# Kernel optimization log

Hardware: AMD Instinct MI355X
Metric: run time of the kernel (lower is better)

The kernel has to match this reference:

```python
import jax, jax.numpy as jnp
import numpy as np

B, S, DIM = 2, 2048, 2048
H, KVH, HD = 16, 8, 128
NREP = H // KVH


def _make_freqs(seqlen, head_dim):
    # Rotation-matrix form of RoPE: freqs[s,0,p] = [[cos,-sin],[sin,cos]]
    pos = jnp.arange(seqlen, dtype=jnp.float32)
    inv = 1.0 / (10000.0 ** (jnp.arange(0, head_dim, 2, dtype=jnp.float32) / head_dim))
    ang = pos[:, None] * inv[None, :]                      # (S, HD/2)
    cos, sin = jnp.cos(ang), jnp.sin(ang)
    f = jnp.stack([jnp.stack([cos, -sin], -1),
                   jnp.stack([sin, cos], -1)], -2)          # (S, HD/2, 2, 2)
    return f[:, None]                                       # (S, 1, HD/2, 2, 2)


def setup_inputs() -> dict:
    key = jax.random.key(0)
    k0, k1, k2, k3, k4 = jax.random.split(key, 5)
    x = jax.random.normal(k0, (B, S, DIM), jnp.float32)
    x_mask = jnp.ones((B, S), jnp.bool_)                    # unused by forward
    freqs_cis = _make_freqs(S, HD)
    w_qkv = jax.random.normal(k1, ((H + 2 * KVH) * HD, DIM), jnp.float32) * (DIM ** -0.5)
    w_out = jax.random.normal(k2, (DIM, H * HD), jnp.float32) * ((H * HD) ** -0.5)
    q_norm_w = 1.0 + 0.02 * jax.random.normal(k3, (HD,), jnp.float32)
    k_norm_w = 1.0 + 0.02 * jax.random.normal(k4, (HD,), jnp.float32)
    return {"x": x, "x_mask": x_mask, "freqs_cis": freqs_cis,
            "w_qkv": w_qkv, "w_out": w_out,
            "q_norm_w": q_norm_w, "k_norm_w": k_norm_w}


def _rmsnorm(x, w):
    eps = jnp.asarray(jnp.finfo(x.dtype).eps, x.dtype)
    return x * jax.lax.rsqrt(jnp.mean(x * x, -1, keepdims=True) + eps) * w


def _rope(x, freqs):
    # x: (B,S,h,HD), freqs: (S,1,HD/2,2,2)
    t = x.reshape(*x.shape[:-1], HD // 2, 1, 2)
    out = freqs[..., 0] * t[..., 0] + freqs[..., 1] * t[..., 1]
    return out.reshape(x.shape)


def reference(x, x_mask, freqs_cis, w_qkv, w_out, q_norm_w, k_norm_w):
    b, s, _ = x.shape
    qkv = jnp.einsum('bsd,od->bso', x, w_qkv)
    xq, xk, xv = jnp.split(qkv, [H * HD, (H + KVH) * HD], axis=-1)
    xq = _rope(_rmsnorm(xq.reshape(b, s, H, HD), q_norm_w), freqs_cis)
    xk = _rope(_rmsnorm(xk.reshape(b, s, KVH, HD), k_norm_w), freqs_cis)
    xv = xv.reshape(b, s, KVH, HD)
    # GQA: repeat kv heads (consecutive copies, matching unsqueeze+repeat+flatten)
    xk = jnp.repeat(xk, NREP, axis=2)
    xv = jnp.repeat(xv, NREP, axis=2)
    scale = HD ** -0.5
    scores = jnp.einsum('bqhd,bkhd->bhqk', xq, xk) * scale
    attn = jax.nn.softmax(scores, axis=-1)
    out = jnp.einsum('bhqk,bkhd->bqhd', attn, xv).reshape(b, s, H * HD)
    return jnp.einsum('bso,do->bsd', out, w_out)
```

## Files before the change

kernel.cpp:

```cpp
#include <hip/hip_runtime.h>
#include <hip/hip_bf16.h>
#include <cstdint>

typedef __bf16 bf16_t;
typedef __attribute__((ext_vector_type(8)))  __bf16 bf16x8;
typedef __attribute__((ext_vector_type(4)))  float  f32x4;
typedef __attribute__((ext_vector_type(16))) float  f32x16;

#define AS1 __attribute__((address_space(1)))
#define AS3 __attribute__((address_space(3)))
#define DEV __device__ __forceinline__

#define S_BARRIER() asm volatile("s_barrier" ::: "memory")
#define VMCNT0()    asm volatile("s_waitcnt vmcnt(0)" ::: "memory")
#define VMCNT8()    asm volatile("s_waitcnt vmcnt(8)" ::: "memory")
#define SCHED0()    __builtin_amdgcn_sched_barrier(0)

#if __has_builtin(__builtin_amdgcn_exp2f)
#define EXP2(x) __builtin_amdgcn_exp2f(x)
#else
#define EXP2(x) exp2f(x)
#endif

DEV uint32_t pk2bf(float lo, float hi) {
  union { __bf16 h[2]; uint32_t u; } x;
  x.h[0] = (__bf16)lo; x.h[1] = (__bf16)hi; return x.u;
}

__global__ __launch_bounds__(256) void k_cvt3(const float* __restrict__ s0,
                                              const float* __restrict__ s1,
                                              const float* __restrict__ s2,
                                              bf16_t* __restrict__ dst) {
  long i = (long)(blockIdx.x * 256 + threadIdx.x) * 4;
  const float* src;
  long off;
  if (i < 8388608)        { src = s0; off = i; }
  else if (i < 16777216)  { src = s1; off = i - 8388608; }
  else                    { src = s2; off = i - 16777216; }
  const float4 v = *reinterpret_cast<const float4*>(src + off);
  union { bf16_t h[4]; uint2 u; } o;
  o.h[0] = (bf16_t)v.x; o.h[1] = (bf16_t)v.y;
  o.h[2] = (bf16_t)v.z; o.h[3] = (bf16_t)v.w;
  *reinterpret_cast<uint2*>(dst + i) = o.u;
}

#define RD_A_PAIR(dst, base, MF)                                          \
  _Pragma("unroll") for (int j_ = 0; j_ < 2; ++j_)                        \
  _Pragma("unroll") for (int kk_ = 0; kk_ < 2; ++kk_) {                   \
    int p_ = (wm*128 + ((MF)+j_)*16 + c16)*128 + kk_*64 + g*16;           \
    p_ ^= ((p_>>9)&1)<<5;                                                 \
    dst[j_][kk_] = *reinterpret_cast<const bf16x8*>((const char*)(base) + p_); }

#define RD_B_ALL(dst, base)                                               \
  _Pragma("unroll") for (int i_ = 0; i_ < 4; ++i_)                        \
  _Pragma("unroll") for (int kk_ = 0; kk_ < 2; ++kk_) {                   \
    int p_ = (wn*64 + i_*16 + c16)*128 + kk_*64 + g*16;                   \
    p_ ^= ((p_>>9)&1)<<5;                                                 \
    dst[i_][kk_] = *reinterpret_cast<const bf16x8*>((const char*)(base) + p_); }

#define RD_B2(dst, base)                                                  \
  _Pragma("unroll") for (int i_ = 0; i_ < 2; ++i_)                        \
  _Pragma("unroll") for (int kk_ = 0; kk_ < 2; ++kk_) {                   \
    int p_ = (wn*32 + i_*16 + c16)*128 + kk_*64 + g*16;                   \
    p_ ^= ((p_>>9)&1)<<5;                                                 \
    dst[i_][kk_] = *reinterpret_cast<const bf16x8*>((const char*)(base) + p_); }

#define MM_PAIR(aa, MF)                                                   \
  _Pragma("unroll") for (int j_ = 0; j_ < 2; ++j_)                        \
  _Pragma("unroll") for (int i_ = 0; i_ < 4; ++i_)                        \
  _Pragma("unroll") for (int kk_ = 0; kk_ < 2; ++kk_)                     \
    acc[(MF)+j_][i_] = __builtin_amdgcn_mfma_f32_16x16x32_bf16(           \
        aa[j_][kk_], bF[i_][kk_], acc[(MF)+j_][i_], 0, 0, 0);

#define MM_PAIR2(aa, MF)                                                  \
  _Pragma("unroll") for (int j_ = 0; j_ < 2; ++j_)                        \
  _Pragma("unroll") for (int i_ = 0; i_ < 2; ++i_)                        \
  _Pragma("unroll") for (int kk_ = 0; kk_ < 2; ++kk_)                     \
    acc[(MF)+j_][i_] = __builtin_amdgcn_mfma_f32_16x16x32_bf16(           \
        aa[j_][kk_], bG[i_][kk_], acc[(MF)+j_][i_], 0, 0, 0);

#define STAGE_A(dstbase, half, tt)                                        \
  _Pragma("unroll") for (int j_ = 0; j_ < 2; ++j_)                        \
    __builtin_amdgcn_global_load_lds(                                     \
        (const AS1 void*)(Ag + srcA[half][j_] + (tt)*64),                 \
        (AS3 void*)((char*)(dstbase) + ((half)*1024 + 512*j_ + wuni)*16), \
        16, 0, 0);

#define STAGE_B(dstbase, half, tt)                                        \
  _Pragma("unroll") for (int j_ = 0; j_ < 2; ++j_)                        \
    __builtin_amdgcn_global_load_lds(                                     \
        (const AS1 void*)(Bg + srcB[half][j_] + (tt)*64),                 \
        (AS3 void*)((char*)(dstbase) + ((half)*1024 + 512*j_ + wuni)*16), \
        16, 0, 0);

#define STAGE_B2(dstbase, tt)                                             \
  _Pragma("unroll") for (int j_ = 0; j_ < 2; ++j_)                        \
    __builtin_amdgcn_global_load_lds(                                     \
        (const AS1 void*)(Bg + srcB2[j_] + (tt)*64),                      \
        (AS3 void*)((char*)(dstbase) + (512*j_ + wuni)*16), 16, 0, 0);

__global__ __launch_bounds__(512, 2) void k_gemm256(
    const bf16_t* __restrict__ Ag, const bf16_t* __restrict__ Bg,
    void* __restrict__ Cv, int M, int N, int K, int out_bf16)
{
  extern __shared__ char smemraw[];
  const int tid = threadIdx.x;
  const int w = tid >> 6, l = tid & 63;
  const int wm = w >> 2, wn = w & 3;
  const int c16 = l & 15, g = l >> 4;
  const int wuni = tid & 0x1C0;

  const int nwg = gridDim.x, cpx = nwg >> 3;
  const int bid = blockIdx.x;
  const int L = (bid & 7) * cpx + (bid >> 3);
  const int nbx = N >> 8;
  const int m0 = (L / nbx) * 256, n0 = (L % nbx) * 256;

  int srcA[2][2], srcB[2][2];
#pragma unroll
  for (int half = 0; half < 2; ++half)
#pragma unroll
    for (int j = 0; j < 2; ++j) {
      int ch = half * 1024 + 512 * j + tid;
      int cc = ch ^ (((ch >> 5) & 1) << 1);
      int row = cc >> 3, c8 = (cc & 7) * 8;
      srcA[half][j] = (m0 + row) * K + c8;
      srcB[half][j] = (n0 + row) * K + c8;
    }

  f32x4 acc[8][4] = {};
  bf16x8 aA[2][2], aB[2][2], bF[4][2];

  char* const Ab0 = smemraw;
  char* const Ab1 = smemraw + 32768;
  char* const Bb0 = smemraw + 65536;
  char* const Bb1 = smemraw + 98304;

  const int NT = K >> 6;

  STAGE_A(Ab0, 0, 0); STAGE_A(Ab0, 1, 0);
  STAGE_B(Bb0, 0, 0); STAGE_B(Bb0, 1, 0);
  VMCNT0();
  S_BARRIER();
  RD_A_PAIR(aA, Ab0, 0);
  RD_B_ALL(bF, Bb0);

#pragma unroll 1
  for (int t = 0; t < NT; ++t) {
    char* const Asp = (t & 1) ? Ab1 : Ab0;
    char* const Asn = (t & 1) ? Ab0 : Ab1;
    char* const Bsn = (t & 1) ? Bb0 : Bb1;
    const bool more = (t + 1 < NT);

    RD_A_PAIR(aB, Asp, 2);
    if (more) { STAGE_A(Asn, 0, t + 1); STAGE_A(Asn, 1, t + 1); }
    S_BARRIER();
    __builtin_amdgcn_s_setprio(1);
    MM_PAIR(aA, 0);
    __builtin_amdgcn_s_setprio(0); SCHED0();
    S_BARRIER();

    RD_A_PAIR(aA, Asp, 4);
    if (more) { STAGE_B(Bsn, 0, t + 1); STAGE_B(Bsn, 1, t + 1); }
    S_BARRIER();
    __builtin_amdgcn_s_setprio(1);
    MM_PAIR(aB, 2);
    __builtin_amdgcn_s_setprio(0); SCHED0();
    S_BARRIER();

    RD_A_PAIR(aB, Asp, 6);
    S_BARRIER();
    __builtin_amdgcn_s_setprio(1);
    MM_PAIR(aA, 4);
    __builtin_amdgcn_s_setprio(0); SCHED0();
    S_BARRIER();

    if (more) { VMCNT0(); }
    S_BARRIER();
    __builtin_amdgcn_s_setprio(1);
    MM_PAIR(aB, 6);
    __builtin_amdgcn_s_setprio(0); SCHED0();
    if (more) { RD_A_PAIR(aA, Asn, 0); RD_B_ALL(bF, Bsn); }
    S_BARRIER();
  }

#pragma unroll
  for (int mf = 0; mf < 8; ++mf)
#pragma unroll
    for (int nf = 0; nf < 4; ++nf) {
      const int cc = n0 + wn * 64 + nf * 16 + c16;
#pragma unroll
      for (int r = 0; r < 4; ++r) {
        const int rr = m0 + wm * 128 + mf * 16 + g * 4 + r;
        if (out_bf16)
          ((bf16_t*)Cv)[(size_t)rr * N + cc] = (bf16_t)acc[mf][nf][r];
        else
          ((float*)Cv)[(size_t)rr * N + cc] = acc[mf][nf][r];
      }
    }
}

__global__ __launch_bounds__(512, 2) void k_og(
    const bf16_t* __restrict__ Ag, const bf16_t* __restrict__ Bg,
    float* __restrict__ Cv, int M, int N, int K)
{
  extern __shared__ char smemraw[];
  const int tid = threadIdx.x;
  const int w = tid >> 6, l = tid & 63;
  const int wm = w >> 2, wn = w & 3;
  const int c16 = l & 15, g = l >> 4;
  const int wuni = tid & 0x1C0;

  const int nwg = gridDim.x, cpx = nwg >> 3;
  const int bid = blockIdx.x;
  const int L = (bid & 7) * cpx + (bid >> 3);
  const int nbx = N >> 7;
  const int m0 = (L / nbx) * 256, n0 = (L % nbx) * 128;

  int srcA[2][2], srcB2[2];
#pragma unroll
  for (int half = 0; half < 2; ++half)
#pragma unroll
    for (int j = 0; j < 2; ++j) {
      int ch = half * 1024 + 512 * j + tid;
      int cc = ch ^ (((ch >> 5) & 1) << 1);
      int row = cc >> 3, c8 = (cc & 7) * 8;
      srcA[half][j] = (m0 + row) * K + c8;
    }
#pragma unroll
  for (int j = 0; j < 2; ++j) {
    int ch = 512 * j + tid;
    int cc = ch ^ (((ch >> 5) & 1) << 1);
    int row = cc >> 3, c8 = (cc & 7) * 8;
    srcB2[j] = (n0 + row) * K + c8;
  }

  f32x4 acc[8][2] = {};
  bf16x8 aA[2][2], aB[2][2], bG[2][2];

  char* const Ab0 = smemraw;
  char* const Ab1 = smemraw + 32768;
  char* const Bb0 = smemraw + 65536;
  char* const Bb1 = smemraw + 81920;

  const int NT = K >> 6;

  STAGE_A(Ab0, 0, 0); STAGE_A(Ab0, 1, 0);
  STAGE_B2(Bb0, 0);
  VMCNT0();
  S_BARRIER();
  RD_A_PAIR(aA, Ab0, 0);
  RD_B2(bG, Bb0);

#pragma unroll 1
  for (int t = 0; t < NT; ++t) {
    char* const Asp = (t & 1) ? Ab1 : Ab0;
    char* const Asn = (t & 1) ? Ab0 : Ab1;
    char* const Bsn = (t & 1) ? Bb0 : Bb1;
    const bool more = (t + 1 < NT);

    RD_A_PAIR(aB, Asp, 2);
    if (more) { STAGE_A(Asn, 0, t + 1); STAGE_A(Asn, 1, t + 1); }
    S_BARRIER();
    __builtin_amdgcn_s_setprio(1);
    MM_PAIR2(aA, 0);
    __builtin_amdgcn_s_setprio(0); SCHED0();
    S_BARRIER();

    RD_A_PAIR(aA, Asp, 4);
    if (more) { STAGE_B2(Bsn, t + 1); }
    S_BARRIER();
    __builtin_amdgcn_s_setprio(1);
    MM_PAIR2(aB, 2);
    __builtin_amdgcn_s_setprio(0); SCHED0();
    S_BARRIER();

    RD_A_PAIR(aB, Asp, 6);
    S_BARRIER();
    __builtin_amdgcn_s_setprio(1);
    MM_PAIR2(aA, 4);
    __builtin_amdgcn_s_setprio(0); SCHED0();
    S_BARRIER();

    if (more) { VMCNT0(); }
    S_BARRIER();
    __builtin_amdgcn_s_setprio(1);
    MM_PAIR2(aB, 6);
    __builtin_amdgcn_s_setprio(0); SCHED0();
    if (more) { RD_A_PAIR(aA, Asn, 0); RD_B2(bG, Bsn); }
    S_BARRIER();
  }

#pragma unroll
  for (int mf = 0; mf < 8; ++mf)
#pragma unroll
    for (int nf = 0; nf < 2; ++nf) {
      const int cc = n0 + wn * 32 + nf * 16 + c16;
#pragma unroll
      for (int r = 0; r < 4; ++r) {
        const int rr = m0 + wm * 128 + mf * 16 + g * 4 + r;
        Cv[(size_t)rr * N + cc] = acc[mf][nf][r];
      }
    }
}

__global__ __launch_bounds__(256) void k_prep(
    const bf16_t* __restrict__ qkv, const float* __restrict__ freqs,
    const float* __restrict__ qw, const float* __restrict__ kw,
    bf16_t* __restrict__ Qd, bf16_t* __restrict__ Kd,
    bf16_t* __restrict__ Vt)
{
  __shared__ bf16_t vt[64][136];
  const int bid = blockIdx.x;
  if (bid < 24576) {
    const int w = threadIdx.x >> 6, l = threadIdx.x & 63;
    const int R = bid * 4 + w;
    const int j = R >> 12;
    const int token = R & 4095;
    const int s = token & 2047, b = token >> 11;
    const bool isq = (j < 16);
    const int col0 = isq ? (j << 7) : (2048 + ((j - 16) << 7));

    union { uint32_t u; __bf16 h[2]; } xin;
    xin.u = *reinterpret_cast<const uint32_t*>(qkv + (size_t)token * 4096 + col0 + 2 * l);
    float x0 = (float)xin.h[0], x1 = (float)xin.h[1];
    float ss = x0 * x0 + x1 * x1;
#pragma unroll
    for (int d = 1; d < 64; d <<= 1) ss += __shfl_xor(ss, d, 64);
    const float rn = rsqrtf(ss * (1.0f / 128.0f) + 1.1920929e-7f);
    const float2 wv = *reinterpret_cast<const float2*>((isq ? qw : kw) + 2 * l);
    const float y0 = x0 * rn * wv.x, y1 = x1 * rn * wv.y;
    const float4 f = *reinterpret_cast<const float4*>(freqs + (size_t)s * 256 + l * 4);
    float o0 = f.x * y0 + f.y * y1;
    float o1 = f.z * y0 + f.w * y1;
    if (isq) { o0 *= 0.1275187989014331f; o1 *= 0.1275187989014331f; }
    const uint32_t pk = pk2bf(o0, o1);
    if (isq)
      *reinterpret_cast<uint32_t*>(Qd + ((size_t)(b * 16 + j) * 2048 + s) * 128 + 2 * l) = pk;
    else
      *reinterpret_cast<uint32_t*>(Kd + ((size_t)(b * 8 + (j - 16)) * 2048 + s) * 128 + 2 * l) = pk;
  } else {
    const int vb = bid - 24576;
    const int tid = threadIdx.x;
    const int st = vb & 31, kh = (vb >> 5) & 7, b = vb >> 8;
    const int s0 = st * 64;
#pragma unroll
    for (int i = 0; i < 4; ++i) {
      int ch = tid + 256 * i;
      int srow = ch >> 4, d8 = ch & 15;
      bf16x8 v = *reinterpret_cast<const bf16x8*>(
          qkv + (size_t)(b * 2048 + s0 + srow) * 4096 + 3072 + kh * 128 + d8 * 8);
      *reinterpret_cast<bf16x8*>(&vt[srow][d8 * 8]) = v;
    }
    __syncthreads();
    const int d = tid >> 1, sc = tid & 1;
    bf16_t* dst = Vt + ((size_t)(b * 8 + kh) * 128 + d) * 2048 + s0 + 32 * sc;
#pragma unroll
    for (int grp = 0; grp < 4; ++grp) {
      uint32_t pk[4];
#pragma unroll
      for (int q = 0; q < 4; ++q) {
        int jj = 32 * sc + grp * 8 + q * 2;
        union { __bf16 h[2]; uint32_t u; } e;
        e.h[0] = vt[jj][d]; e.h[1] = vt[jj + 1][d];
        pk[q] = e.u;
      }
      uint4 o; o.x = pk[0]; o.y = pk[1]; o.z = pk[2]; o.w = pk[3];
      *reinterpret_cast<uint4*>(dst + grp * 8) = o;
    }
  }
}

__global__ __launch_bounds__(256, 2) void k_attn(
    const bf16_t* __restrict__ Qd, const bf16_t* __restrict__ Kd,
    const bf16_t* __restrict__ Vt, bf16_t* __restrict__ O)
{
  __shared__ bf16_t kbuf[2][64 * 128];
  __shared__ bf16_t vbuf[2][128 * 64];
  const int tid = threadIdx.x;
  const int w = tid >> 6, l = tid & 63;
  const int c = l & 31, h2 = l >> 5;
  const int bid = blockIdx.x;
  const int qt = bid & 15, h = (bid >> 4) & 15, b = bid >> 8;
  const int kvh = h >> 1;
  const bf16_t* Qg = Qd + ((size_t)(b * 16 + h) * 2048 + qt * 128 + w * 32) * 128;
  const bf16_t* Kg = Kd + ((size_t)(b * 8 + kvh) * 2048) * 128;
  const bf16_t* Vg = Vt + ((size_t)(b * 8 + kvh) * 128) * 2048;

  bf16x8 qf[8];
#pragma unroll
  for (int s = 0; s < 8; ++s)
    qf[s] = *reinterpret_cast<const bf16x8*>(Qg + (size_t)c * 128 + s * 16 + h2 * 8);

  f32x16 oacc[4] = {};
  float l0 = 0.f, l1 = 0.f, l2 = 0.f, l3 = 0.f;

  auto stage = [&](int buf, int kt) {
#pragma unroll
    for (int i = 0; i < 4; ++i) {
      int ch = tid + 256 * i;
      {
        int key = ch >> 4, d16 = ch & 15;
        int soff = key * 256 + ((d16 * 16) ^ ((key & 7) << 4));
        __builtin_amdgcn_global_load_lds(
            (const AS1 void*)((const char*)Kg + (size_t)kt * 64 * 256 + soff),
            (AS3 void*)((char*)&kbuf[buf][0] + (w * 64 + 256 * i) * 16), 16, 0, 0);
      }
      {
        int d = ch >> 3, k8 = (ch & 7) ^ (d & 7);
        __builtin_amdgcn_global_load_lds(
            (const AS1 void*)(Vg + (size_t)d * 2048 + kt * 64 + k8 * 8),
            (AS3 void*)((char*)&vbuf[buf][0] + (w * 64 + 256 * i) * 16), 16, 0, 0);
      }
    }
  };

  auto compute = [&](int buf) {
    f32x16 sacc[2] = {};
    const char* kb = (const char*)&kbuf[buf][0];
    __builtin_amdgcn_s_setprio(1);
#pragma unroll
    for (int m = 0; m < 2; ++m)
#pragma unroll
      for (int s = 0; s < 8; ++s) {
        int byte = (m * 32 + c) * 256 + ((s * 32 + h2 * 16) ^ ((c & 7) << 4));
        bf16x8 kf = *reinterpret_cast<const bf16x8*>(kb + byte);
        sacc[m] = __builtin_amdgcn_mfma_f32_32x32x16_bf16(kf, qf[s], sacc[m], 0, 0, 0);
      }
    __builtin_amdgcn_s_setprio(0);

#pragma unroll
    for (int m = 0; m < 2; ++m)
#pragma unroll
      for (int r = 0; r < 16; r += 4) {
        float p0 = EXP2(sacc[m][r + 0]);
        float p1 = EXP2(sacc[m][r + 1]);
        float p2 = EXP2(sacc[m][r + 2]);
        float p3 = EXP2(sacc[m][r + 3]);
        sacc[m][r + 0] = p0; sacc[m][r + 1] = p1;
        sacc[m][r + 2] = p2; sacc[m][r + 3] = p3;
        l0 += p0; l1 += p1; l2 += p2; l3 += p3;
      }

    const char* vb = (const char*)&vbuf[buf][0];
#pragma unroll
    for (int t = 0; t < 4; ++t) {
      const int m = t >> 1, q2i = t & 1;
      uint32_t u0 = pk2bf(sacc[m][8 * q2i + 0], sacc[m][8 * q2i + 1]);
      uint32_t u1 = pk2bf(sacc[m][8 * q2i + 2], sacc[m][8 * q2i + 3]);
      uint32_t u2 = pk2bf(sacc[m][8 * q2i + 4], sacc[m][8 * q2i + 5]);
      uint32_t u3 = pk2bf(sacc[m][8 * q2i + 6], sacc[m][8 * q2i + 7]);
      auto r02 = __builtin_amdgcn_permlane32_swap((int)u0, (int)u2, false, false);
      auto r13 = __builtin_amdgcn_permlane32_swap((int)u1, (int)u3, false, false);
      union { uint32_t u[4]; bf16x8 v; } pb;
      pb.u[0] = (uint32_t)r02[0]; pb.u[1] = (uint32_t)r13[0];
      pb.u[2] = (uint32_t)r02[1]; pb.u[3] = (uint32_t)r13[1];
      __builtin_amdgcn_s_setprio(1);
#pragma unroll
      for (int df = 0; df < 4; ++df) {
        int byte = (df * 32 + c) * 128 + ((t * 32 + h2 * 16) ^ ((c & 7) << 4));
        bf16x8 vf = *reinterpret_cast<const bf16x8*>(vb + byte);
        oacc[df] = __builtin_amdgcn_mfma_f32_32x32x16_bf16(vf, pb.v, oacc[df], 0, 0, 0);
      }
      __builtin_amdgcn_s_setprio(0);
    }
  };

  stage(0, 0);
#pragma unroll 1
  for (int kt = 0; kt < 31; ++kt) {
    stage((kt + 1) & 1, kt + 1);
    VMCNT8();
    S_BARRIER();
    compute(kt & 1);
    S_BARRIER();
  }
  VMCNT0();
  S_BARRIER();
  compute(1);

  float lrun = (l0 + l1) + (l2 + l3);
  lrun += __shfl_xor(lrun, 32, 64);
  const float inv = 1.0f / lrun;
  bf16_t* Og = O + ((size_t)(b * 2048 + qt * 128 + w * 32 + c) * 2048) + h * 128;
#pragma unroll
  for (int df = 0; df < 4; ++df)
#pragma unroll
    for (int rg = 0; rg < 4; ++rg) {
      uint32_t w0 = pk2bf(oacc[df][rg * 4 + 0] * inv, oacc[df][rg * 4 + 1] * inv);
      uint32_t w1 = pk2bf(oacc[df][rg * 4 + 2] * inv, oacc[df][rg * 4 + 3] * inv);
      uint2 ww; ww.x = w0; ww.y = w1;
      *reinterpret_cast<uint2*>(Og + df * 32 + 8 * rg + 4 * h2) = ww;
    }
}

extern "C" void kernel_launch(void* const* d_in, const int* in_sizes, int n_in,
                              void* d_out, int out_size, void* d_ws, size_t ws_size,
                              hipStream_t stream)
{
  const float* x     = (const float*)d_in[0];
  const float* freqs = (const float*)d_in[2];
  const float* wqkv  = (const float*)d_in[3];
  const float* wout  = (const float*)d_in[4];
  const float* qw    = (const float*)d_in[5];
  const float* kw    = (const float*)d_in[6];
  float* out = (float*)d_out;

  bf16_t* Xb   = (bf16_t*)d_ws;
  bf16_t* Wqb  = Xb  + 8388608;
  bf16_t* Wob  = Wqb + 8388608;
  bf16_t* qkvb = Wob + 4194304;
  bf16_t* Qdp  = qkvb + 16777216;
  bf16_t* Kdp  = Qdp + 8388608;
  bf16_t* Vtp  = Kdp + 4194304;
  bf16_t* Ob   = qkvb;

  (void)hipFuncSetAttribute((const void*)k_gemm256,
                            hipFuncAttributeMaxDynamicSharedMemorySize, 131072);
  (void)hipFuncSetAttribute((const void*)k_og,
                            hipFuncAttributeMaxDynamicSharedMemorySize, 98304);

  k_cvt3<<<20480, 256, 0, stream>>>(x, wqkv, wout, Xb);
  k_gemm256<<<256, 512, 131072, stream>>>(Xb, Wqb, qkvb, 4096, 4096, 2048, 1);
  k_prep<<<25088, 256, 0, stream>>>(qkvb, freqs, qw, kw, Qdp, Kdp, Vtp);
  k_attn<<<512, 256, 0, stream>>>(Qdp, Kdp, Vtp, Ob);
  k_og<<<256, 512, 98304, stream>>>(Ob, Wob, out, 4096, 2048, 2048);
}
```

Baseline: 230.0 us.

## Restructure GEMM main loops into quadrant MFMA phases with staggered staging

Both bf16 GEMM kernels now read four A fragments at a time and issue MFMAs in quadrant blocks (4x2) instead of row pairs. Global-to-LDS staging is split across phases: B first, then A halves, with a partial vmcnt wait. The output GEMM drops from four to two phases per k-tile, which removes barriers. The goal is fewer barriers and better overlap of loads with MFMA work. The cost is more registers for A fragments and LDS reads that are no longer double-buffered in registers, so they now sit on the critical path before each MFMA block.

```diff
diff --git a/kernel.cpp b/kernel.cpp
--- a/kernel.cpp
+++ b/kernel.cpp
@@ -13,6 +13,7 @@
 
 #define S_BARRIER() asm volatile("s_barrier" ::: "memory")
 #define VMCNT0()    asm volatile("s_waitcnt vmcnt(0)" ::: "memory")
+#define VMCNT4()    asm volatile("s_waitcnt vmcnt(4)" ::: "memory")
 #define VMCNT8()    asm volatile("s_waitcnt vmcnt(8)" ::: "memory")
 #define SCHED0()    __builtin_amdgcn_sched_barrier(0)
 
@@ -44,8 +45,8 @@
   *reinterpret_cast<uint2*>(dst + i) = o.u;
 }
 
-#define RD_A_PAIR(dst, base, MF)                                          \
-  _Pragma("unroll") for (int j_ = 0; j_ < 2; ++j_)                        \
+#define RD_A4(dst, base, MF)                                              \
+  _Pragma("unroll") for (int j_ = 0; j_ < 4; ++j_)                        \
   _Pragma("unroll") for (int kk_ = 0; kk_ < 2; ++kk_) {                   \
     int p_ = (wm*128 + ((MF)+j_)*16 + c16)*128 + kk_*64 + g*16;           \
     p_ ^= ((p_>>9)&1)<<5;                                                 \
@@ -65,19 +66,19 @@
     p_ ^= ((p_>>9)&1)<<5;                                                 \
     dst[i_][kk_] = *reinterpret_cast<const bf16x8*>((const char*)(base) + p_); }
 
-#define MM_PAIR(aa, MF)                                                   \
-  _Pragma("unroll") for (int j_ = 0; j_ < 2; ++j_)                        \
-  _Pragma("unroll") for (int i_ = 0; i_ < 4; ++i_)                        \
-  _Pragma("unroll") for (int kk_ = 0; kk_ < 2; ++kk_)                     \
-    acc[(MF)+j_][i_] = __builtin_amdgcn_mfma_f32_16x16x32_bf16(           \
-        aa[j_][kk_], bF[i_][kk_], acc[(MF)+j_][i_], 0, 0, 0);
-
-#define MM_PAIR2(aa, MF)                                                  \
-  _Pragma("unroll") for (int j_ = 0; j_ < 2; ++j_)                        \
+#define MM_Q(aa, MB, NB)                                                  \
+  _Pragma("unroll") for (int j_ = 0; j_ < 4; ++j_)                        \
   _Pragma("unroll") for (int i_ = 0; i_ < 2; ++i_)                        \
   _Pragma("unroll") for (int kk_ = 0; kk_ < 2; ++kk_)                     \
-    acc[(MF)+j_][i_] = __builtin_amdgcn_mfma_f32_16x16x32_bf16(           \
-        aa[j_][kk_], bG[i_][kk_], acc[(MF)+j_][i_], 0, 0, 0);
+    acc[(MB)+j_][(NB)+i_] = __builtin_amdgcn_mfma_f32_16x16x32_bf16(      \
+        aa[j_][kk_], bF[(NB)+i_][kk_], acc[(MB)+j_][(NB)+i_], 0, 0, 0);
+
+#define MM_OG(aa, MB)                                                     \
+  _Pragma("unroll") for (int j_ = 0; j_ < 4; ++j_)                        \
+  _Pragma("unroll") for (int i_ = 0; i_ < 2; ++i_)                        \
+  _Pragma("unroll") for (int kk_ = 0; kk_ < 2; ++kk_)                     \
+    acc[(MB)+j_][i_] = __builtin_amdgcn_mfma_f32_16x16x32_bf16(           \
+        aa[j_][kk_], bG[i_][kk_], acc[(MB)+j_][i_], 0, 0, 0);
 
 #define STAGE_A(dstbase, half, tt)                                        \
   _Pragma("unroll") for (int j_ = 0; j_ < 2; ++j_)                        \
@@ -129,7 +130,7 @@
     }
 
   f32x4 acc[8][4] = {};
-  bf16x8 aA[2][2], aB[2][2], bF[4][2];
+  bf16x8 aF[4][2], bF[4][2];
 
   char* const Ab0 = smemraw;
   char* const Ab1 = smemraw + 32768;
@@ -138,11 +139,10 @@
 
   const int NT = K >> 6;
 
+  STAGE_B(Bb0, 0, 0); STAGE_B(Bb0, 1, 0);
   STAGE_A(Ab0, 0, 0); STAGE_A(Ab0, 1, 0);
-  STAGE_B(Bb0, 0, 0); STAGE_B(Bb0, 1, 0);
   VMCNT0();
   S_BARRIER();
-  RD_A_PAIR(aA, Ab0, 0);
   RD_B_ALL(bF, Bb0);
 
 #pragma unroll 1
@@ -152,35 +152,36 @@
     char* const Bsn = (t & 1) ? Bb0 : Bb1;
     const bool more = (t + 1 < NT);
 
-    RD_A_PAIR(aB, Asp, 2);
-    if (more) { STAGE_A(Asn, 0, t + 1); STAGE_A(Asn, 1, t + 1); }
-    S_BARRIER();
-    __builtin_amdgcn_s_setprio(1);
-    MM_PAIR(aA, 0);
+    VMCNT0();
+    if (more) { STAGE_B(Bsn, 0, t + 1); }
+    S_BARRIER();
+    RD_A4(aF, Asp, 0);
+    __builtin_amdgcn_s_setprio(1);
+    MM_Q(aF, 0, 0);
     __builtin_amdgcn_s_setprio(0); SCHED0();
     S_BARRIER();
 
-    RD_A_PAIR(aA, Asp, 4);
-    if (more) { STAGE_B(Bsn, 0, t + 1); STAGE_B(Bsn, 1, t + 1); }
-    S_BARRIER();
-    __builtin_amdgcn_s_setprio(1);
-    MM_PAIR(aB, 2);
+    if (more) { STAGE_B(Bsn, 1, t + 1); }
+    S_BARRIER();
+    __builtin_amdgcn_s_setprio(1);
+    MM_Q(aF, 0, 2);
     __builtin_amdgcn_s_setprio(0); SCHED0();
     S_BARRIER();
 
-    RD_A_PAIR(aB, Asp, 6);
-    S_BARRIER();
-    __builtin_amdgcn_s_setprio(1);
-    MM_PAIR(aA, 4);
+    if (more) { STAGE_A(Asn, 0, t + 1); }
+    S_BARRIER();
+    RD_A4(aF, Asp, 4);
+    __builtin_amdgcn_s_setprio(1);
+    MM_Q(aF, 4, 0);
     __builtin_amdgcn_s_setprio(0); SCHED0();
     S_BARRIER();
 
-    if (more) { VMCNT0(); }
-    S_BARRIER();
-    __builtin_amdgcn_s_setprio(1);
-    MM_PAIR(aB, 6);
+    if (more) { STAGE_A(Asn, 1, t + 1); VMCNT4(); }
+    S_BARRIER();
+    __builtin_amdgcn_s_setprio(1);
+    MM_Q(aF, 4, 2);
     __builtin_amdgcn_s_setprio(0); SCHED0();
-    if (more) { RD_A_PAIR(aA, Asn, 0); RD_B_ALL(bF, Bsn); }
+    if (more) { RD_B_ALL(bF, Bsn); }
     S_BARRIER();
   }
 
@@ -236,7 +237,7 @@
   }
 
   f32x4 acc[8][2] = {};
-  bf16x8 aA[2][2], aB[2][2], bG[2][2];
+  bf16x8 aF[4][2], bG[2][2];
 
   char* const Ab0 = smemraw;
   char* const Ab1 = smemraw + 32768;
@@ -245,11 +246,10 @@
 
   const int NT = K >> 6;
 
+  STAGE_B2(Bb0, 0);
   STAGE_A(Ab0, 0, 0); STAGE_A(Ab0, 1, 0);
-  STAGE_B2(Bb0, 0);
   VMCNT0();
   S_BARRIER();
-  RD_A_PAIR(aA, Ab0, 0);
   RD_B2(bG, Bb0);
 
 #pragma unroll 1
@@ -259,35 +259,22 @@
     char* const Bsn = (t & 1) ? Bb0 : Bb1;
     const bool more = (t + 1 < NT);
 
-    RD_A_PAIR(aB, Asp, 2);
-    if (more) { STAGE_A(Asn, 0, t + 1); STAGE_A(Asn, 1, t + 1); }
-    S_BARRIER();
-    __builtin_amdgcn_s_setprio(1);
-    MM_PAIR2(aA, 0);
+    VMCNT0();
+    if (more) { STAGE_B2(Bsn, t + 1); STAGE_A(Asn, 0, t + 1); }
+    S_BARRIER();
+    RD_A4(aF, Asp, 0);
+    __builtin_amdgcn_s_setprio(1);
+    MM_OG(aF, 0);
     __builtin_amdgcn_s_setprio(0); SCHED0();
     S_BARRIER();
 
-    RD_A_PAIR(aA, Asp, 4);
-    if (more) { STAGE_B2(Bsn, t + 1); }
-    S_BARRIER();
-    __builtin_amdgcn_s_setprio(1);
-    MM_PAIR2(aB, 2);
+    if (more) { STAGE_A(Asn, 1, t + 1); VMCNT4(); }
+    S_BARRIER();
+    RD_A4(aF, Asp, 4);
+    __builtin_amdgcn_s_setprio(1);
+    MM_OG(aF, 4);
     __builtin_amdgcn_s_setprio(0); SCHED0();
-    S_BARRIER();
-
-    RD_A_PAIR(aB, Asp, 6);
-    S_BARRIER();
-    __builtin_amdgcn_s_setprio(1);
-    MM_PAIR2(aA, 4);
-    __builtin_amdgcn_s_setprio(0); SCHED0();
-    S_BARRIER();
-
-    if (more) { VMCNT0(); }
-    S_BARRIER();
-    __builtin_amdgcn_s_setprio(1);
-    MM_PAIR2(aB, 6);
-    __builtin_amdgcn_s_setprio(0); SCHED0();
-    if (more) { RD_A_PAIR(aA, Asn, 0); RD_B2(bG, Bsn); }
+    if (more) { RD_B2(bG, Bsn); }
     S_BARRIER();
   }
 
```

Measured after the change: 232.8 us. No clear change (+1.2%).
